# Optimization experiments

Hardware: AMD Instinct MI355X
Metric: run time of the kernel (lower is better)

## Reference

```python
import jax, jax.numpy as jnp
import numpy as np

EPS = 1e-5

def rmsnorm(x, w):
    var = jnp.mean(x * x, axis=-1, keepdims=True)
    return x * jax.lax.rsqrt(var + EPS) * w


def setup_inputs() -> dict:
    key = jax.random.key(0)
    B, L, dim = 4, 2048, 1024
    d_inner, d_state, d_conv, dt_rank = 2 * dim, 16, 4, dim // 16
    ks = jax.random.split(key, 8)
    g = lambda k, shape, scale: (jax.random.normal(k, shape, jnp.float32) * scale)
    return {
        "x": g(ks[0], (B, L, dim), 1.0),
        "rms_w": jnp.ones((dim,), jnp.float32),
        "in_proj": g(ks[1], (dim, 2 * d_inner), dim ** -0.5),
        "conv_w": g(ks[2], (d_inner, d_conv), 0.25),
        "conv_b": jnp.zeros((d_inner,), jnp.float32),
        "x_proj": g(ks[3], (d_inner, dt_rank + 2 * d_state), d_inner ** -0.5),
        "dt_w": g(ks[4], (dt_rank, d_inner), dt_rank ** -0.5),
        # inverse-softplus(0.01): softplus(dt_b) ~ 0.01 at init, standard Mamba dt init
        "dt_b": jnp.full((d_inner,), float(np.log(np.expm1(0.01))), jnp.float32),
        # S4D-real init: A_n = -(n+1)
        "A_log": jnp.log(jnp.broadcast_to(jnp.arange(1, d_state + 1, dtype=jnp.float32), (d_inner, d_state))).copy(),
        "D": jnp.ones((d_inner,), jnp.float32),
        "out_proj": g(ks[5], (d_inner, dim), d_inner ** -0.5),
    }


def _mamba_block(x, rms_w, in_proj, conv_w, conv_b, x_proj, dt_w, dt_b, A_log, D, out_proj):
    B, L, dim = x.shape
    d_inner, K = conv_w.shape
    d_state = A_log.shape[1]
    dt_rank = dt_w.shape[0]

    xn = rmsnorm(x, rms_w)
    xz = xn @ in_proj                      # [B,L,2*d_inner]
    xi, z = jnp.split(xz, 2, axis=-1)

    # causal depthwise conv1d over L
    xc = jax.lax.conv_general_dilated(
        xi.transpose(0, 2, 1),             # [B,C,L]
        conv_w[:, None, :],                # [C,1,K]
        window_strides=(1,), padding=[(K - 1, 0)],
        feature_group_count=d_inner,
    ).transpose(0, 2, 1) + conv_b
    xi = jax.nn.silu(xc)                   # [B,L,d_inner]

    dbc = xi @ x_proj                      # [B,L,dt_rank+2*d_state]
    dt, Bm, Cm = jnp.split(dbc, [dt_rank, dt_rank + d_state], axis=-1)
    delta = jax.nn.softplus(dt @ dt_w + dt_b)  # [B,L,d_inner]
    A = -jnp.exp(A_log)                    # [d_inner,d_state]

    def step(h, inputs):
        d_t, x_t, B_t, C_t = inputs        # [B,d_inner],[B,d_inner],[B,d_state],[B,d_state]
        dA = jnp.exp(d_t[..., None] * A)   # [B,d_inner,d_state]
        h = dA * h + (d_t * x_t)[..., None] * B_t[:, None, :]
        y = jnp.einsum('bds,bs->bd', h, C_t)
        return h, y

    h0 = jnp.zeros((B, d_inner, d_state), x.dtype)
    xs = (delta.transpose(1, 0, 2), xi.transpose(1, 0, 2),
          Bm.transpose(1, 0, 2), Cm.transpose(1, 0, 2))
    _, ys = jax.lax.scan(step, h0, xs)     # ys: [L,B,d_inner]

    y = ys.transpose(1, 0, 2) + xi * D     # D skip connection
    y = y * jax.nn.silu(z)                 # output gate
    return x + y @ out_proj                # residual


def reference(x, rms_w, in_proj, conv_w, conv_b, x_proj, dt_w, dt_b, A_log, D, out_proj):
    return _mamba_block(x, rms_w, in_proj, conv_w, conv_b, x_proj, dt_w, dt_b, A_log, D, out_proj)
```

## Files before the change

### kernel.cpp

```cpp
#include <hip/hip_runtime.h>
#include <hip/hip_bf16.h>
#include <math.h>


#define ROWS 8192
#define DIM 1024
#define DINNER 2048
#define DSTATE 16
#define DTRANK 64
#define LSEQ 2048
#define NCHUNK 32
#define LCHUNK 64

#define LOG2E 1.4426950408889634f

typedef unsigned short ushort;
typedef __attribute__((ext_vector_type(8))) short short8;
typedef __attribute__((ext_vector_type(4))) float float4v;

__device__ inline ushort f2bf(float f) {
    __hip_bfloat16 h = __float2bfloat16(f);
    return *reinterpret_cast<ushort*>(&h);
}
__device__ inline float bf2f(ushort u) {
    union { unsigned int i; float f; } w; w.i = ((unsigned int)u) << 16; return w.f;
}

__device__ inline float fexp2(float x) {
#if __has_builtin(__builtin_amdgcn_exp2f)
    return __builtin_amdgcn_exp2f(x);
#else
    return __expf(x * 0.69314718056f);
#endif
}

__device__ inline void dma16(const void* g, void* l) {
    __builtin_amdgcn_global_load_lds(
        (const __attribute__((address_space(1))) unsigned int*)g,
        (__attribute__((address_space(3))) unsigned int*)l, 16, 0, 0);
}

template <int N> __device__ inline void vwait() {
    if constexpr (N == 0)      asm volatile("s_waitcnt vmcnt(0)" ::: "memory");
    else if constexpr (N == 4) asm volatile("s_waitcnt vmcnt(4)" ::: "memory");
    else if constexpr (N == 6) asm volatile("s_waitcnt vmcnt(6)" ::: "memory");
    else if constexpr (N == 8) asm volatile("s_waitcnt vmcnt(8)" ::: "memory");
    else if constexpr (N == 12) asm volatile("s_waitcnt vmcnt(12)" ::: "memory");
    else static_assert(N < 0, "unsupported vmcnt literal");
}

__global__ __launch_bounds__(256)
void prep_kernel(const float* __restrict__ in_proj, ushort* __restrict__ bt1,
                 const float* __restrict__ out_proj, ushort* __restrict__ bt2,
                 const float* __restrict__ x_proj, ushort* __restrict__ bt3,
                 const float* __restrict__ dt_w, ushort* __restrict__ bt4,
                 const float* __restrict__ x, const float* __restrict__ rms_w,
                 ushort* __restrict__ xn, float* __restrict__ dbc) {
    __shared__ float tld[32][33];
    __shared__ float red[4];
    int bid = blockIdx.x, tid = threadIdx.x;
    if (bid < 6464) {
        const float* in; ushort* outT; int R, C, bx, by;
        if (bid < 4096)      { in = in_proj;  outT = bt1; R = 1024; C = 4096; bx = bid & 127; by = bid >> 7; }
        else if (bid < 6144) { int t = bid - 4096; in = out_proj; outT = bt2; R = 2048; C = 1024; bx = t & 31; by = t >> 5; }
        else if (bid < 6336) { int t = bid - 6144; in = x_proj;  outT = bt3; R = 2048; C = 96;  bx = t % 3;  by = t / 3; }
        else                 { int t = bid - 6336; in = dt_w;    outT = bt4; R = 64;   C = 2048; bx = t & 63; by = t >> 6; }
        int tx = tid & 31, ty = tid >> 5;
#pragma unroll
        for (int k = 0; k < 4; ++k)
            tld[ty + k * 8][tx] = in[(long)(by * 32 + ty + k * 8) * C + bx * 32 + tx];
        __syncthreads();
#pragma unroll
        for (int k = 0; k < 4; ++k)
            outT[(long)(bx * 32 + ty + k * 8) * R + by * 32 + tx] = f2bf(tld[tx][ty + k * 8]);
    } else if (bid < 14656) {
        int row = bid - 6464;
        float4 xv = ((const float4*)(x + (long)row * DIM))[tid];
        float ss = xv.x * xv.x + xv.y * xv.y + xv.z * xv.z + xv.w * xv.w;
        for (int off = 32; off > 0; off >>= 1) ss += __shfl_down(ss, off);
        if ((tid & 63) == 0) red[tid >> 6] = ss;
        __syncthreads();
        float scale = rsqrtf((red[0] + red[1] + red[2] + red[3]) / DIM + 1e-5f);
        float4 wv = ((const float4*)rms_w)[tid];
        ushort4 ov;
        ov.x = f2bf(xv.x * scale * wv.x);
        ov.y = f2bf(xv.y * scale * wv.y);
        ov.z = f2bf(xv.z * scale * wv.z);
        ov.w = f2bf(xv.w * scale * wv.w);
        ((ushort4*)xn)[(long)row * 256 + tid] = ov;
    } else {
        int idx = (bid - 14656) * 256 + tid;
        float4 z = {0.f, 0.f, 0.f, 0.f};
        ((float4*)dbc)[idx] = z;
    }
}

template <int MW, int NW, int MF, int NF, int EPI>
__global__ __launch_bounds__(MW * NW * 64, 2)
void gemm_ring(const ushort* __restrict__ A, int lda,
               const ushort* __restrict__ Bt, int ldbt,
               void* __restrict__ Cv, int ldc, int K,
               const float* __restrict__ aux) {
    constexpr int W    = MW * NW;
    constexpr int BLKM = MW * MF * 16;
    constexpr int BLKN = NW * NF * 16;
    constexpr int TILE = (BLKM + BLKN) * 32;
    constexpr int NA   = BLKM / (16 * W);
    constexpr int NB   = BLKN / (16 * W);
    constexpr int DPT  = NA + NB;
    constexpr int MH   = MF / 2;
    __shared__ __align__(16) ushort lds[3 * TILE];

    const int nwg = gridDim.x * gridDim.y;
    int bid = blockIdx.y * gridDim.x + blockIdx.x;
    bid = (bid & 7) * (nwg >> 3) + (bid >> 3);
    const int bx = bid % gridDim.x;
    const int by = bid / gridDim.x;

    const int tid  = threadIdx.x;
    const int w    = tid >> 6, lane = tid & 63;
    const int wm   = w / NW,   wn   = w % NW;
    const int quad = lane >> 4, l16 = lane & 15;
    const long row0 = (long)by * BLKM;
    const long col0 = (long)bx * BLKN;

    const ushort* gA[NA];
    const ushort* gB[NB];
#pragma unroll
    for (int i = 0; i < NA; ++i)
        gA[i] = A + (row0 + (w + i * W) * 16 + l16) * lda + quad * 8;
#pragma unroll
    for (int i = 0; i < NB; ++i)
        gB[i] = Bt + (col0 + (w + i * W) * 16 + l16) * ldbt + quad * 8;

    const int NT = K >> 5;
    float4v acc[MF][NF] = {};

    auto stageA = [&](int kt, int slot) {
        ushort* lb = lds + slot * TILE;
        const int ko = kt << 5;
#pragma unroll
        for (int i = 0; i < NA; ++i)
            dma16(gA[i] + ko, lb + (w + i * W) * 512);
    };
    auto stageB = [&](int kt, int slot) {
        ushort* lb = lds + slot * TILE + BLKM * 32;
        const int ko = kt << 5;
#pragma unroll
        for (int i = 0; i < NB; ++i)
            dma16(gB[i] + ko, lb + (w + i * W) * 512);
    };

    stageA(0, 0); stageB(0, 0); stageA(1, 1); stageB(1, 1);
    vwait<DPT>();
    __builtin_amdgcn_s_barrier();

    int s = 0;
    for (int t = 0; t < NT; ++t) {
        const ushort* lb  = lds + s * TILE;
        const ushort* lbB = lb + BLKM * 32;
        const bool stg = (t + 2 < NT);
        const int ss = (s >= 1) ? s - 1 : 2;
        short8 af[MF], bfr[NF];

#pragma unroll
        for (int n = 0; n < NF; ++n)
            bfr[n] = *reinterpret_cast<const short8*>(
                &lbB[(wn * NF + n) * 512 + lane * 8]);
#pragma unroll
        for (int m = 0; m < MH; ++m)
            af[m] = *reinterpret_cast<const short8*>(
                &lb[(wm * MF + m) * 512 + lane * 8]);
        if (stg) stageA(t + 2, ss);
        __builtin_amdgcn_s_barrier();
        asm volatile("s_waitcnt lgkmcnt(0)" ::: "memory");
        __builtin_amdgcn_sched_barrier(0);
        __builtin_amdgcn_s_setprio(1);
#pragma unroll
        for (int m = 0; m < MH; ++m)
#pragma unroll
            for (int n = 0; n < NF; ++n)
                acc[m][n] = __builtin_amdgcn_mfma_f32_16x16x32_bf16(
                    af[m], bfr[n], acc[m][n], 0, 0, 0);
        __builtin_amdgcn_s_setprio(0);
        __builtin_amdgcn_s_barrier();

#pragma unroll
        for (int m = MH; m < MF; ++m)
            af[m] = *reinterpret_cast<const short8*>(
                &lb[(wm * MF + m) * 512 + lane * 8]);
        if (stg) stageB(t + 2, ss);
        __builtin_amdgcn_s_barrier();
        asm volatile("s_waitcnt lgkmcnt(0)" ::: "memory");
        __builtin_amdgcn_sched_barrier(0);
        __builtin_amdgcn_s_setprio(1);
#pragma unroll
        for (int m = MH; m < MF; ++m)
#pragma unroll
            for (int n = 0; n < NF; ++n)
                acc[m][n] = __builtin_amdgcn_mfma_f32_16x16x32_bf16(
                    af[m], bfr[n], acc[m][n], 0, 0, 0);
        __builtin_amdgcn_s_setprio(0);
        if (stg) vwait<DPT>(); else vwait<0>();
        if (t < NT - 1) __builtin_amdgcn_s_barrier();
        s = (s == 2) ? 0 : s + 1;
    }

#pragma unroll
    for (int m = 0; m < MF; ++m) {
#pragma unroll
        for (int n = 0; n < NF; ++n) {
            long rbase = row0 + wm * (MF * 16) + m * 16 + quad * 4;
            long c = col0 + wn * (NF * 16) + n * 16 + l16;
#pragma unroll
            for (int r = 0; r < 4; ++r) {
                float v = acc[m][n][r];
                long idx = (rbase + r) * (long)ldc + c;
                if (EPI == 2) ((float*)Cv)[idx] = v + aux[idx];
                else          ((ushort*)Cv)[idx] = f2bf(v);
            }
        }
    }
}

__global__ __launch_bounds__(256)
void xproj_conv_gemm(const ushort* __restrict__ xz,
                     const float* __restrict__ cw, const float* __restrict__ cb,
                     const ushort* __restrict__ bt3,
                     float* __restrict__ dbc) {
    __shared__ __align__(16) ushort As[128][32];
    __shared__ __align__(16) ushort Bs[128][32];
    int tid = threadIdx.x;
    int wave = tid >> 6, lane = tid & 63;
    int wm = wave >> 1, wn = wave & 1;
    int quad = lane >> 4, l16 = lane & 15;
    int row0 = blockIdx.y * 128;
    int ks0 = blockIdx.x * 512;
    int srow = tid >> 2, sseg = tid & 3;

    int r0 = (wave * 2 + 0) * 16 + (lane >> 2);
    int r1 = (wave * 2 + 1) * 16 + (lane >> 2);
    int ksl = (lane & 3) * 8;
    const ushort* b0 = bt3 + (long)r0 * 2048 + ks0 + ksl;
    const ushort* b1 = bt3 + (long)r1 * 2048 + ks0 + ksl;
    ushort* lB0 = &Bs[(wave * 2 + 0) * 16][0];
    ushort* lB1 = &Bs[(wave * 2 + 1) * 16][0];

    float4v acc[4][4] = {};

    for (int k0 = 0; k0 < 512; k0 += 32) {
        dma16(b0 + k0, lB0);
        dma16(b1 + k0, lB1);
#pragma unroll
        for (int it = 0; it < 2; ++it) {
            int r = srow + it * 64;
            long row = row0 + r;
            int l = (int)(row & (LSEQ - 1));
            int cch = ks0 + k0 + sseg * 8;
            short8 v[4];
#pragma unroll
            for (int t = 0; t < 4; ++t) {
                if (l - 3 + t >= 0) v[t] = *(const short8*)&xz[(row - 3 + t) * 4096 + cch];
                else { short8 zz = {0,0,0,0,0,0,0,0}; v[t] = zz; }
            }
            ushort o[8];
#pragma unroll
            for (int j = 0; j < 8; ++j) {
                float4 w = ((const float4*)cw)[cch + j];
                float a = cb[cch + j]
                        + bf2f((ushort)v[0][j]) * w.x + bf2f((ushort)v[1][j]) * w.y
                        + bf2f((ushort)v[2][j]) * w.z + bf2f((ushort)v[3][j]) * w.w;
                a = a / (1.f + __expf(-a));
                o[j] = f2bf(a);
            }
            *(short8*)&As[r][sseg * 8] = *(const short8*)o;
        }
        __syncthreads();

        short8 afrag[4], bfrag[4];
#pragma unroll
        for (int i = 0; i < 4; ++i)
            afrag[i] = *reinterpret_cast<const short8*>(&As[wm * 64 + i * 16 + l16][quad * 8]);
#pragma unroll
        for (int j = 0; j < 4; ++j)
            bfrag[j] = *reinterpret_cast<const short8*>(&Bs[wn * 64 + j * 16 + l16][quad * 8]);
#pragma unroll
        for (int i = 0; i < 4; ++i)
#pragma unroll
            for (int j = 0; j < 4; ++j)
                acc[i][j] = __builtin_amdgcn_mfma_f32_16x16x32_bf16(
                    afrag[i], bfrag[j], acc[i][j], 0, 0, 0);
        __syncthreads();
    }
#pragma unroll
    for (int i = 0; i < 4; ++i) {
#pragma unroll
        for (int j = 0; j < 4; ++j) {
            int rbase = row0 + wm * 64 + i * 16 + quad * 4;
            int c = wn * 64 + j * 16 + l16;
            if (c < 96) {
#pragma unroll
                for (int r = 0; r < 4; ++r)
                    atomicAdd(&dbc[(long)(rbase + r) * 96 + c], acc[i][j][r]);
            }
        }
    }
}

__global__ __launch_bounds__(256)
void mfma_gemm_dt(const float* __restrict__ A, int lda,
                  const ushort* __restrict__ Bt, int ldbt,
                  ushort* __restrict__ C, int ldc, int K,
                  const float* __restrict__ aux) {
    __shared__ __align__(16) ushort As[128][40];
    __shared__ __align__(16) ushort Bs[128][40];
    int tid = threadIdx.x;
    int wave = tid >> 6, lane = tid & 63;
    int wm = wave >> 1, wn = wave & 1;
    int quad = lane >> 4, l16 = lane & 15;
    int row0 = blockIdx.y * 128, col0 = blockIdx.x * 128;
    int srow = tid >> 2, sseg = tid & 3;

    float4v acc[4][4] = {};

    for (int k0 = 0; k0 < K; k0 += 32) {
#pragma unroll
        for (int it = 0; it < 2; ++it) {
            int r = srow + it * 64;
            const float* ap = A + (long)(row0 + r) * lda + k0 + sseg * 8;
            ushort tmp[8];
#pragma unroll
            for (int j = 0; j < 8; ++j) tmp[j] = f2bf(ap[j]);
            *reinterpret_cast<short8*>(&As[r][sseg * 8]) =
                *reinterpret_cast<const short8*>(tmp);
            const ushort* bp = Bt + (long)(col0 + r) * ldbt + k0 + sseg * 8;
            *reinterpret_cast<short8*>(&Bs[r][sseg * 8]) =
                *reinterpret_cast<const short8*>(bp);
        }
        __syncthreads();
        short8 afrag[4], bfrag[4];
#pragma unroll
        for (int i = 0; i < 4; ++i)
            afrag[i] = *reinterpret_cast<const short8*>(&As[wm * 64 + i * 16 + l16][quad * 8]);
#pragma unroll
        for (int j = 0; j < 4; ++j)
            bfrag[j] = *reinterpret_cast<const short8*>(&Bs[wn * 64 + j * 16 + l16][quad * 8]);
#pragma unroll
        for (int i = 0; i < 4; ++i)
#pragma unroll
            for (int j = 0; j < 4; ++j)
                acc[i][j] = __builtin_amdgcn_mfma_f32_16x16x32_bf16(
                    afrag[i], bfrag[j], acc[i][j], 0, 0, 0);
        __syncthreads();
    }
#pragma unroll
    for (int i = 0; i < 4; ++i) {
#pragma unroll
        for (int j = 0; j < 4; ++j) {
            int rbase = row0 + wm * 64 + i * 16 + quad * 4;
            int c = col0 + wn * 64 + j * 16 + l16;
#pragma unroll
            for (int r = 0; r < 4; ++r) {
                float v = acc[i][j][r] + aux[c];
                v = (v > 20.f) ? v : __logf(1.f + __expf(v));
                C[(long)(rbase + r) * ldc + c] = f2bf(v);
            }
        }
    }
}

__global__ __launch_bounds__(256)
void scan_part1(const ushort* __restrict__ xz,
                const ushort* __restrict__ dlt,
                const float* __restrict__ dbc,
                const float* __restrict__ A_log,
                const float* __restrict__ cw, const float* __restrict__ cb,
                float* __restrict__ hbuf,
                float* __restrict__ sdbuf) {
    int c = blockIdx.y * 256 + threadIdx.x;
    int b = blockIdx.z, g = blockIdx.x;
    float A2[16];
#pragma unroll
    for (int s = 0; s < 16; ++s) A2[s] = -__expf(A_log[c * 16 + s]) * LOG2E;
    float4 w = ((const float4*)cw)[c];
    float cbc = cb[c];
    float h[16] = {};
    float sumd = 0.f;
    long row0 = (long)b * LSEQ + (long)g * LCHUNK;
    int l0 = g * LCHUNK;
    float x0 = (l0 >= 3) ? bf2f(xz[(row0 - 3) * 4096 + c]) : 0.f;
    float x1 = (l0 >= 2) ? bf2f(xz[(row0 - 2) * 4096 + c]) : 0.f;
    float x2 = (l0 >= 1) ? bf2f(xz[(row0 - 1) * 4096 + c]) : 0.f;
    long row = row0;
    for (int l = 0; l < LCHUNK; ++l, ++row) {
        float x3 = bf2f(xz[row * 4096 + c]);
        float xc = cbc + x0 * w.x + x1 * w.y + x2 * w.z + x3 * w.w;
        xc = xc / (1.f + __expf(-xc));
        x0 = x1; x1 = x2; x2 = x3;
        float d = bf2f(dlt[row * 2048 + c]);
        const float* __restrict__ bc = dbc + row * 96;
        sumd += d;
        float dx = d * xc;
#pragma unroll
        for (int s = 0; s < 16; ++s)
            h[s] = fexp2(d * A2[s]) * h[s] + dx * bc[64 + s];
    }
    long hb = ((long)(b * NCHUNK + g) * 16) * 2048 + c;
#pragma unroll
    for (int s = 0; s < 16; ++s) hbuf[hb + (long)s * 2048] = h[s];
    sdbuf[(long)(b * NCHUNK + g) * 2048 + c] = sumd;
}

__global__ __launch_bounds__(256)
void scan_part2(float* __restrict__ hbuf, const float* __restrict__ sdbuf,
                const float* __restrict__ A_log) {
    int gl = blockIdx.x * 256 + threadIdx.x;
    int c = gl & 2047, s = (gl >> 11) & 15, b = gl >> 15;
    float A2 = -__expf(A_log[c * 16 + s]) * LOG2E;
    float hrun = 0.f;
    for (int g = 0; g < NCHUNK; ++g) {
        long hi = ((long)(b * NCHUNK + g) * 16 + s) * 2048 + c;
        float hout = hbuf[hi];
        float sd = sdbuf[(long)(b * NCHUNK + g) * 2048 + c];
        hbuf[hi] = hrun;
        hrun = fexp2(A2 * sd) * hrun + hout;
    }
}

__global__ __launch_bounds__(256)
void scan_part3(const ushort* __restrict__ xz,
                ushort* __restrict__ dlt,
                const float* __restrict__ dbc,
                const float* __restrict__ A_log,
                const float* __restrict__ cw, const float* __restrict__ cb,
                const float* __restrict__ Dp,
                const float* __restrict__ hbuf) {
    int c = blockIdx.y * 256 + threadIdx.x;
    int b = blockIdx.z, g = blockIdx.x;
    float A2[16], h[16];
#pragma unroll
    for (int s = 0; s < 16; ++s) A2[s] = -__expf(A_log[c * 16 + s]) * LOG2E;
    long hb = ((long)(b * NCHUNK + g) * 16) * 2048 + c;
#pragma unroll
    for (int s = 0; s < 16; ++s) h[s] = hbuf[hb + (long)s * 2048];
    float4 w = ((const float4*)cw)[c];
    float cbc = cb[c];
    float Dc = Dp[c];
    long row0 = (long)b * LSEQ + (long)g * LCHUNK;
    int l0 = g * LCHUNK;
    float x0 = (l0 >= 3) ? bf2f(xz[(row0 - 3) * 4096 + c]) : 0.f;
    float x1 = (l0 >= 2) ? bf2f(xz[(row0 - 2) * 4096 + c]) : 0.f;
    float x2 = (l0 >= 1) ? bf2f(xz[(row0 - 1) * 4096 + c]) : 0.f;
    long row = row0;
    for (int l = 0; l < LCHUNK; ++l, ++row) {
        float x3 = bf2f(xz[row * 4096 + c]);
        float xc = cbc + x0 * w.x + x1 * w.y + x2 * w.z + x3 * w.w;
        xc = xc / (1.f + __expf(-xc));
        x0 = x1; x1 = x2; x2 = x3;
        float d = bf2f(dlt[row * 2048 + c]);
        float z = bf2f(xz[row * 4096 + 2048 + c]);
        const float* __restrict__ bc = dbc + row * 96;
        float dx = d * xc;
        float y = 0.f;
#pragma unroll
        for (int s = 0; s < 16; ++s) {
            h[s] = fexp2(d * A2[s]) * h[s] + dx * bc[64 + s];
            y += h[s] * bc[80 + s];
        }
        float yv = (y + xc * Dc) * (z / (1.f + __expf(-z)));
        dlt[row * 2048 + c] = f2bf(yv);
    }
}

extern "C" void kernel_launch(void* const* d_in, const int* in_sizes, int n_in,
                              void* d_out, int out_size, void* d_ws, size_t ws_size,
                              hipStream_t stream) {
    const float* x        = (const float*)d_in[0];
    const float* rms_w    = (const float*)d_in[1];
    const float* in_proj  = (const float*)d_in[2];
    const float* conv_w   = (const float*)d_in[3];
    const float* conv_b   = (const float*)d_in[4];
    const float* x_proj   = (const float*)d_in[5];
    const float* dt_w     = (const float*)d_in[6];
    const float* dt_b     = (const float*)d_in[7];
    const float* A_log    = (const float*)d_in[8];
    const float* Dp       = (const float*)d_in[9];
    const float* out_proj = (const float*)d_in[10];
    float* out = (float*)d_out;

    char* p = (char*)d_ws;
    ushort* xz  = (ushort*)p;   p += (size_t)ROWS * 4096 * 2;
    ushort* dlt = (ushort*)p;   p += (size_t)ROWS * 2048 * 2;
    float*  dbc = (float*)p;    p += (size_t)ROWS * 96 * 4;
    ushort* bt1 = (ushort*)p;   p += (size_t)4096 * 1024 * 2;
    ushort* bt2 = (ushort*)p;   p += (size_t)1024 * 2048 * 2;
    ushort* bt3 = (ushort*)p;   p += (size_t)128 * 2048 * 2;
    ushort* bt4 = (ushort*)p;   p += (size_t)2048 * 64 * 2;
    ushort* xn  = (ushort*)p;   p += (size_t)ROWS * 1024 * 2;
    float* sdbuf = (float*)p;   p += (size_t)4 * NCHUNK * 2048 * 4;
    float* hbuf  = (float*)xn;

    prep_kernel<<<15424, 256, 0, stream>>>(in_proj, bt1, out_proj, bt2,
                                           x_proj, bt3, dt_w, bt4,
                                           x, rms_w, xn, dbc);
    gemm_ring<1, 4, 8, 4, 0><<<dim3(4096 / 256, ROWS / 128), 256, 0, stream>>>(
        xn, DIM, bt1, 1024, xz, 4096, DIM, nullptr);
    xproj_conv_gemm<<<dim3(4, ROWS / 128), 256, 0, stream>>>(
        xz, conv_w, conv_b, bt3, dbc);
    mfma_gemm_dt<<<dim3(2048 / 128, ROWS / 128), 256, 0, stream>>>(
        dbc, 96, bt4, 64, dlt, 2048, DTRANK, dt_b);
    scan_part1<<<dim3(NCHUNK, DINNER / 256, 4), 256, 0, stream>>>(
        xz, dlt, dbc, A_log, conv_w, conv_b, hbuf, sdbuf);
    scan_part2<<<512, 256, 0, stream>>>(hbuf, sdbuf, A_log);
    scan_part3<<<dim3(NCHUNK, DINNER / 256, 4), 256, 0, stream>>>(
        xz, dlt, dbc, A_log, conv_w, conv_b, Dp, hbuf);
    gemm_ring<1, 4, 8, 4, 2><<<dim3(DIM / 256, ROWS / 128), 256, 0, stream>>>(
        dlt, DINNER, bt2, DINNER, out, DIM, DINNER, x);
}
```

Baseline: 495.0 us.

## Simplify GEMM to double-buffer, retile launches, replace dbc atomics with partial-sum reduce

The GEMM kernel drops its triple-buffered split A/B staging, split MFMA halves and XCD-aware block swizzle in favour of a simple double-buffered loop with 8 waves per block and a higher occupancy hint. The in_proj and out_proj GEMM launches are retiled to 512-thread blocks with different wave and fragment shapes. The x_proj GEMM now writes per-column-block partial sums to scratch (reusing the xn buffer), and a new reduce kernel sums them, replacing float atomics and the zero-fill in prep. Dropping the deeper pipeline and the swizzle may expose more load latency and lose L2 locality, in exchange for higher occupancy.

```diff
diff --git a/kernel.cpp b/kernel.cpp
--- a/kernel.cpp
+++ b/kernel.cpp
@@ -42,10 +42,9 @@
 
 template <int N> __device__ inline void vwait() {
     if constexpr (N == 0)      asm volatile("s_waitcnt vmcnt(0)" ::: "memory");
+    else if constexpr (N == 3) asm volatile("s_waitcnt vmcnt(3)" ::: "memory");
     else if constexpr (N == 4) asm volatile("s_waitcnt vmcnt(4)" ::: "memory");
     else if constexpr (N == 6) asm volatile("s_waitcnt vmcnt(6)" ::: "memory");
-    else if constexpr (N == 8) asm volatile("s_waitcnt vmcnt(8)" ::: "memory");
-    else if constexpr (N == 12) asm volatile("s_waitcnt vmcnt(12)" ::: "memory");
     else static_assert(N < 0, "unsupported vmcnt literal");
 }
 
@@ -55,7 +54,7 @@
                  const float* __restrict__ x_proj, ushort* __restrict__ bt3,
                  const float* __restrict__ dt_w, ushort* __restrict__ bt4,
                  const float* __restrict__ x, const float* __restrict__ rms_w,
-                 ushort* __restrict__ xn, float* __restrict__ dbc) {
+                 ushort* __restrict__ xn) {
     __shared__ float tld[32][33];
     __shared__ float red[4];
     int bid = blockIdx.x, tid = threadIdx.x;
@@ -73,7 +72,7 @@
 #pragma unroll
         for (int k = 0; k < 4; ++k)
             outT[(long)(bx * 32 + ty + k * 8) * R + by * 32 + tx] = f2bf(tld[tx][ty + k * 8]);
-    } else if (bid < 14656) {
+    } else {
         int row = bid - 6464;
         float4 xv = ((const float4*)(x + (long)row * DIM))[tid];
         float ss = xv.x * xv.x + xv.y * xv.y + xv.z * xv.z + xv.w * xv.w;
@@ -88,15 +87,11 @@
         ov.z = f2bf(xv.z * scale * wv.z);
         ov.w = f2bf(xv.w * scale * wv.w);
         ((ushort4*)xn)[(long)row * 256 + tid] = ov;
-    } else {
-        int idx = (bid - 14656) * 256 + tid;
-        float4 z = {0.f, 0.f, 0.f, 0.f};
-        ((float4*)dbc)[idx] = z;
     }
 }
 
 template <int MW, int NW, int MF, int NF, int EPI>
-__global__ __launch_bounds__(MW * NW * 64, 2)
+__global__ __launch_bounds__(MW * NW * 64, 4)
 void gemm_ring(const ushort* __restrict__ A, int lda,
                const ushort* __restrict__ Bt, int ldbt,
                void* __restrict__ Cv, int ldc, int K,
@@ -107,22 +102,14 @@
     constexpr int TILE = (BLKM + BLKN) * 32;
     constexpr int NA   = BLKM / (16 * W);
     constexpr int NB   = BLKN / (16 * W);
-    constexpr int DPT  = NA + NB;
-    constexpr int MH   = MF / 2;
-    __shared__ __align__(16) ushort lds[3 * TILE];
-
-    const int nwg = gridDim.x * gridDim.y;
-    int bid = blockIdx.y * gridDim.x + blockIdx.x;
-    bid = (bid & 7) * (nwg >> 3) + (bid >> 3);
-    const int bx = bid % gridDim.x;
-    const int by = bid / gridDim.x;
+    __shared__ __align__(16) ushort lds[2 * TILE];
 
     const int tid  = threadIdx.x;
     const int w    = tid >> 6, lane = tid & 63;
     const int wm   = w / NW,   wn   = w % NW;
     const int quad = lane >> 4, l16 = lane & 15;
-    const long row0 = (long)by * BLKM;
-    const long col0 = (long)bx * BLKN;
+    const long row0 = (long)blockIdx.y * BLKM;
+    const long col0 = (long)blockIdx.x * BLKN;
 
     const ushort* gA[NA];
     const ushort* gB[NB];
@@ -136,74 +123,45 @@
     const int NT = K >> 5;
     float4v acc[MF][NF] = {};
 
-    auto stageA = [&](int kt, int slot) {
+    auto stage = [&](int kt, int slot) {
         ushort* lb = lds + slot * TILE;
         const int ko = kt << 5;
 #pragma unroll
         for (int i = 0; i < NA; ++i)
             dma16(gA[i] + ko, lb + (w + i * W) * 512);
+#pragma unroll
+        for (int i = 0; i < NB; ++i)
+            dma16(gB[i] + ko, lb + BLKM * 32 + (w + i * W) * 512);
     };
-    auto stageB = [&](int kt, int slot) {
-        ushort* lb = lds + slot * TILE + BLKM * 32;
-        const int ko = kt << 5;
-#pragma unroll
-        for (int i = 0; i < NB; ++i)
-            dma16(gB[i] + ko, lb + (w + i * W) * 512);
-    };
-
-    stageA(0, 0); stageB(0, 0); stageA(1, 1); stageB(1, 1);
-    vwait<DPT>();
+
+    stage(0, 0);
+    vwait<0>();
     __builtin_amdgcn_s_barrier();
 
-    int s = 0;
     for (int t = 0; t < NT; ++t) {
+        const int s = t & 1;
+        if (t + 1 < NT) stage(t + 1, s ^ 1);
         const ushort* lb  = lds + s * TILE;
         const ushort* lbB = lb + BLKM * 32;
-        const bool stg = (t + 2 < NT);
-        const int ss = (s >= 1) ? s - 1 : 2;
         short8 af[MF], bfr[NF];
-
+#pragma unroll
+        for (int m = 0; m < MF; ++m)
+            af[m] = *reinterpret_cast<const short8*>(
+                &lb[(wm * MF + m) * 512 + lane * 8]);
 #pragma unroll
         for (int n = 0; n < NF; ++n)
             bfr[n] = *reinterpret_cast<const short8*>(
                 &lbB[(wn * NF + n) * 512 + lane * 8]);
-#pragma unroll
-        for (int m = 0; m < MH; ++m)
-            af[m] = *reinterpret_cast<const short8*>(
-                &lb[(wm * MF + m) * 512 + lane * 8]);
-        if (stg) stageA(t + 2, ss);
-        __builtin_amdgcn_s_barrier();
-        asm volatile("s_waitcnt lgkmcnt(0)" ::: "memory");
-        __builtin_amdgcn_sched_barrier(0);
         __builtin_amdgcn_s_setprio(1);
 #pragma unroll
-        for (int m = 0; m < MH; ++m)
+        for (int m = 0; m < MF; ++m)
 #pragma unroll
             for (int n = 0; n < NF; ++n)
                 acc[m][n] = __builtin_amdgcn_mfma_f32_16x16x32_bf16(
                     af[m], bfr[n], acc[m][n], 0, 0, 0);
         __builtin_amdgcn_s_setprio(0);
-        __builtin_amdgcn_s_barrier();
-
-#pragma unroll
-        for (int m = MH; m < MF; ++m)
-            af[m] = *reinterpret_cast<const short8*>(
-                &lb[(wm * MF + m) * 512 + lane * 8]);
-        if (stg) stageB(t + 2, ss);
-        __builtin_amdgcn_s_barrier();
-        asm volatile("s_waitcnt lgkmcnt(0)" ::: "memory");
-        __builtin_amdgcn_sched_barrier(0);
-        __builtin_amdgcn_s_setprio(1);
-#pragma unroll
-        for (int m = MH; m < MF; ++m)
-#pragma unroll
-            for (int n = 0; n < NF; ++n)
-                acc[m][n] = __builtin_amdgcn_mfma_f32_16x16x32_bf16(
-                    af[m], bfr[n], acc[m][n], 0, 0, 0);
-        __builtin_amdgcn_s_setprio(0);
-        if (stg) vwait<DPT>(); else vwait<0>();
+        vwait<0>();
         if (t < NT - 1) __builtin_amdgcn_s_barrier();
-        s = (s == 2) ? 0 : s + 1;
     }
 
 #pragma unroll
@@ -227,7 +185,7 @@
 void xproj_conv_gemm(const ushort* __restrict__ xz,
                      const float* __restrict__ cw, const float* __restrict__ cb,
                      const ushort* __restrict__ bt3,
-                     float* __restrict__ dbc) {
+                     float* __restrict__ dbcp) {
     __shared__ __align__(16) ushort As[128][32];
     __shared__ __align__(16) ushort Bs[128][32];
     int tid = threadIdx.x;
@@ -292,6 +250,7 @@
                     afrag[i], bfrag[j], acc[i][j], 0, 0, 0);
         __syncthreads();
     }
+    float* dst = dbcp + (long)blockIdx.x * ROWS * 96;
 #pragma unroll
     for (int i = 0; i < 4; ++i) {
 #pragma unroll
@@ -301,10 +260,25 @@
             if (c < 96) {
 #pragma unroll
                 for (int r = 0; r < 4; ++r)
-                    atomicAdd(&dbc[(long)(rbase + r) * 96 + c], acc[i][j][r]);
+                    dst[(long)(rbase + r) * 96 + c] = acc[i][j][r];
             }
         }
     }
+}
+
+__global__ __launch_bounds__(256)
+void dbc_reduce(const float4* __restrict__ dbcp, float4* __restrict__ dbc) {
+    int i = blockIdx.x * 256 + threadIdx.x;
+    float4 a = dbcp[i];
+    float4 b = dbcp[i + 196608];
+    float4 c = dbcp[i + 2 * 196608];
+    float4 d = dbcp[i + 3 * 196608];
+    float4 o;
+    o.x = a.x + b.x + c.x + d.x;
+    o.y = a.y + b.y + c.y + d.y;
+    o.z = a.z + b.z + c.z + d.z;
+    o.w = a.w + b.w + c.w + d.w;
+    dbc[i] = o;
 }
 
 __global__ __launch_bounds__(256)
@@ -499,14 +473,16 @@
     ushort* xn  = (ushort*)p;   p += (size_t)ROWS * 1024 * 2;
     float* sdbuf = (float*)p;   p += (size_t)4 * NCHUNK * 2048 * 4;
     float* hbuf  = (float*)xn;
-
-    prep_kernel<<<15424, 256, 0, stream>>>(in_proj, bt1, out_proj, bt2,
+    float* dbcp  = (float*)xn;
+
+    prep_kernel<<<14656, 256, 0, stream>>>(in_proj, bt1, out_proj, bt2,
                                            x_proj, bt3, dt_w, bt4,
-                                           x, rms_w, xn, dbc);
-    gemm_ring<1, 4, 8, 4, 0><<<dim3(4096 / 256, ROWS / 128), 256, 0, stream>>>(
+                                           x, rms_w, xn);
+    gemm_ring<2, 4, 4, 4, 0><<<dim3(4096 / 256, ROWS / 128), 512, 0, stream>>>(
         xn, DIM, bt1, 1024, xz, 4096, DIM, nullptr);
     xproj_conv_gemm<<<dim3(4, ROWS / 128), 256, 0, stream>>>(
-        xz, conv_w, conv_b, bt3, dbc);
+        xz, conv_w, conv_b, bt3, dbcp);
+    dbc_reduce<<<768, 256, 0, stream>>>((const float4*)dbcp, (float4*)dbc);
     mfma_gemm_dt<<<dim3(2048 / 128, ROWS / 128), 256, 0, stream>>>(
         dbc, 96, bt4, 64, dlt, 2048, DTRANK, dt_b);
     scan_part1<<<dim3(NCHUNK, DINNER / 256, 4), 256, 0, stream>>>(
@@ -514,6 +490,6 @@
     scan_part2<<<512, 256, 0, stream>>>(hbuf, sdbuf, A_log);
     scan_part3<<<dim3(NCHUNK, DINNER / 256, 4), 256, 0, stream>>>(
         xz, dlt, dbc, A_log, conv_w, conv_b, Dp, hbuf);
-    gemm_ring<1, 4, 8, 4, 2><<<dim3(DIM / 256, ROWS / 128), 256, 0, stream>>>(
+    gemm_ring<4, 2, 2, 4, 2><<<dim3(DIM / 128, ROWS / 128), 512, 0, stream>>>(
         dlt, DINNER, bt2, DINNER, out, DIM, DINNER, x);
 }
```

Result: slower. 509.6 us (+2.9%).
